# Optimization experiments

Measured on AMD Instinct MI355X. Metric: run time of the kernel, lower is better.

The kernel has to match this reference:

```python
import jax, jax.numpy as jnp
import numpy as np

B, M, N, K = 256, 512, 256, 16


def setup_inputs() -> dict:
    key = jax.random.key(0)
    k1, k2, k3, k4 = jax.random.split(key, 4)
    x = jax.random.normal(k1, (B, M, N), dtype=jnp.float32)
    # Linear(in_features=N, out_features=1): weight [1, N], bias [1]
    w_weight = jax.random.normal(k2, (1, N), dtype=jnp.float32) * (2.0 / (N + 1)) ** 0.5
    w_bias = jnp.zeros((1,), dtype=jnp.float32)
    # v: [N, K], xavier_normal
    v = jax.random.normal(k3, (N, K), dtype=jnp.float32) * (2.0 / (N + K)) ** 0.5
    return {"x": x, "w_weight": w_weight, "w_bias": w_bias, "v": v}


def reference(x, w_weight, w_bias, v):
    # Linear term: [B, M, 1]
    l = x @ w_weight.T + w_bias  # broadcasts bias [1]
    # Pairwise interaction. Original: result[b,a,c] = x[b,a] @ (V V^T) @ x[b,c]
    # p[b,a] = 0.5 * (sum_c result[b,a,c] - result[b,a,a])
    # Efficient O(B*M*K) identity: with xv = x @ V,
    #   sum_c result[b,a,c] = xv[b,a] . sum_c xv[b,c]
    #   result[b,a,a]       = ||xv[b,a]||^2
    xv = jnp.einsum('bmn,nk->bmk', x, v)        # [B, M, K]
    sv = xv.sum(axis=1)                          # [B, K]
    row_sum = jnp.einsum('bmk,bk->bm', xv, sv)  # [B, M]
    diag = jnp.sum(xv * xv, axis=-1)             # [B, M]
    p = 0.5 * (row_sum - diag)                   # [B, M]
    return l + p[..., None]                      # [B, M, 1]
```

## Files before the change

### kernel.cpp

```cpp
#include <hip/hip_runtime.h>

#define B_ 256
#define M_ 512
#define N_ 256
#define K_ 16
#define TR 64
#define NT 4

typedef __attribute__((ext_vector_type(8))) short short8;
typedef __attribute__((ext_vector_type(4))) float f32x4;

__device__ __forceinline__ unsigned short f2bf(float f) {
    unsigned u = __builtin_bit_cast(unsigned, f);
    u += 0x7FFFu + ((u >> 16) & 1u);
    return (unsigned short)(u >> 16);
}
__device__ __forceinline__ float bf2f(unsigned short h) {
    unsigned u = ((unsigned)h) << 16;
    return __builtin_bit_cast(float, u);
}

__global__ __launch_bounds__(256) void fm_pass1(
    const float* __restrict__ x, const float* __restrict__ w,
    const float* __restrict__ bias, const float* __restrict__ v,
    unsigned short* __restrict__ xvb, float* __restrict__ svpart,
    float* __restrict__ out)
{
    __shared__ __align__(16) unsigned char xL[2][TR * 512];
    __shared__ __align__(16) unsigned short wLb[N_];
    __shared__ __align__(16) float red[64];

    const int t   = threadIdx.x;
    const int l   = t & 63;
    const int wv  = t >> 6;
    const int blk = blockIdx.x;
    const int b   = blk >> 1;
    const int m0  = (blk & 1) * (NT * TR);
    const float bias0 = bias[0];

    if (t < 64) {
        float4 wq = *(const float4*)(w + t * 4);
        wLb[t * 4 + 0] = f2bf(wq.x); wLb[t * 4 + 1] = f2bf(wq.y);
        wLb[t * 4 + 2] = f2bf(wq.z); wLb[t * 4 + 3] = f2bf(wq.w);
    }

    short8 vB[8];
    #pragma unroll
    for (int c = 0; c < 8; ++c) {
        #pragma unroll
        for (int j = 0; j < 8; ++j) {
            float f = v[(size_t)(c * 32 + (l >> 4) * 8 + j) * K_ + (l & 15)];
            vB[c][j] = (short)f2bf(f);
        }
    }

    const float* gx = x + (size_t)(b * M_ + m0) * N_;

    const int swq = l >> 1;
    const int shf = (l & 1) * 8;

    float4 st[16];
    #pragma unroll
    for (int j = 0; j < 16; ++j)
        st[j] = *(const float4*)(gx + j * 1024 + t * 4);
    #pragma unroll
    for (int j = 0; j < 16; ++j) {
        const int row = j * 4 + wv;
        unsigned lo = (unsigned)f2bf(st[j].x) | ((unsigned)f2bf(st[j].y) << 16);
        unsigned hi = (unsigned)f2bf(st[j].z) | ((unsigned)f2bf(st[j].w) << 16);
        unsigned* d = (unsigned*)(xL[0] + row * 512 + ((swq ^ (row & 7)) << 4) + shf);
        d[0] = lo; d[1] = hi;
    }
    __syncthreads();

    f32x4 acc[NT];
    #pragma unroll
    for (int T = 0; T < NT; ++T) acc[T] = f32x4{0.f, 0.f, 0.f, 0.f};

    #pragma unroll
    for (int T = 0; T < NT; ++T) {
        const int cur = T & 1;
        if (T + 1 < NT) {
            #pragma unroll
            for (int j = 0; j < 16; ++j)
                st[j] = *(const float4*)(gx + (size_t)(T + 1) * TR * N_ + j * 1024 + t * 4);
        }

        const int arow = wv * 16 + (l & 15);
        const unsigned char* abase = xL[cur] + arow * 512;
        #pragma unroll
        for (int c = 0; c < 8; ++c) {
            short8 a = *(const short8*)(abase + (((c * 4 + (l >> 4)) ^ (arow & 7)) << 4));
            acc[T] = __builtin_amdgcn_mfma_f32_16x16x32_bf16(a, vB[c], acc[T], 0, 0, 0);
        }

        {
            const int row = t >> 2;
            const int qt  = t & 3;
            const unsigned char* rbase = xL[cur] + row * 512;
            float ls = 0.f;
            #pragma unroll
            for (int i = 0; i < 8; ++i) {
                short8 xs = *(const short8*)(rbase + ((((qt * 8 + i)) ^ (row & 7)) << 4));
                short8 ws = *(const short8*)((const unsigned char*)wLb + qt * 128 + i * 16);
                #pragma unroll
                for (int e = 0; e < 8; ++e)
                    ls += bf2f((unsigned short)xs[e]) * bf2f((unsigned short)ws[e]);
            }
            ls += __shfl_xor(ls, 1);
            ls += __shfl_xor(ls, 2);
            if (qt == 0)
                out[(size_t)b * M_ + m0 + T * TR + row] = ls + bias0;
        }

        if (T + 1 < NT) {
            #pragma unroll
            for (int j = 0; j < 16; ++j) {
                const int row = j * 4 + wv;
                unsigned lo = (unsigned)f2bf(st[j].x) | ((unsigned)f2bf(st[j].y) << 16);
                unsigned hi = (unsigned)f2bf(st[j].z) | ((unsigned)f2bf(st[j].w) << 16);
                unsigned* d = (unsigned*)(xL[cur ^ 1] + row * 512 + ((swq ^ (row & 7)) << 4) + shf);
                d[0] = lo; d[1] = hi;
            }
        }
        __syncthreads();
    }

    #pragma unroll
    for (int T = 0; T < NT; ++T) {
        const int rbase = m0 + T * TR + wv * 16 + (l >> 4) * 4;
        #pragma unroll
        for (int r = 0; r < 4; ++r)
            xvb[(size_t)(b * M_ + rbase + r) * K_ + (l & 15)] = f2bf(acc[T][r]);
    }

    float s = 0.f;
    #pragma unroll
    for (int T = 0; T < NT; ++T)
        s += acc[T][0] + acc[T][1] + acc[T][2] + acc[T][3];
    s += __shfl_xor(s, 16);
    s += __shfl_xor(s, 32);
    if (l < 16) red[wv * 16 + l] = s;
    __syncthreads();
    if (t < 16)
        svpart[(size_t)blk * 16 + t] = red[t] + red[16 + t] + red[32 + t] + red[48 + t];
}

__global__ __launch_bounds__(256) void fm_pass2(
    const unsigned short* __restrict__ xvb, const float* __restrict__ svpart,
    float* __restrict__ out)
{
    const int t = threadIdx.x;
    const int blk = blockIdx.x;
    const int b = blk >> 1;
    const int m = (blk & 1) * 256 + t;
    __shared__ __align__(16) float svL[16];
    if (t < 16)
        svL[t] = svpart[(size_t)(b * 2 + 0) * 16 + t] + svpart[(size_t)(b * 2 + 1) * 16 + t];
    __syncthreads();

    const unsigned short* xp = xvb + ((size_t)b * M_ + m) * K_;
    short8 h0 = *(const short8*)(xp);
    short8 h1 = *(const short8*)(xp + 8);

    float rs = 0.f, dg = 0.f;
    #pragma unroll
    for (int k = 0; k < 8; ++k) {
        const float a = bf2f((unsigned short)h0[k]);
        rs += a * svL[k];
        dg += a * a;
    }
    #pragma unroll
    for (int k = 0; k < 8; ++k) {
        const float a = bf2f((unsigned short)h1[k]);
        rs += a * svL[8 + k];
        dg += a * a;
    }

    const size_t o = (size_t)b * M_ + m;
    out[o] = out[o] + 0.5f * (rs - dg);
}

extern "C" void kernel_launch(void* const* d_in, const int* in_sizes, int n_in,
                              void* d_out, int out_size, void* d_ws, size_t ws_size,
                              hipStream_t stream) {
    const float* x    = (const float*)d_in[0];
    const float* w    = (const float*)d_in[1];
    const float* bias = (const float*)d_in[2];
    const float* v    = (const float*)d_in[3];
    float* out = (float*)d_out;

    unsigned short* xvb = (unsigned short*)d_ws;
    float* svpart = (float*)((char*)d_ws + ((size_t)B_ * M_ * K_ * 2));

    fm_pass1<<<dim3(B_ * 2), dim3(256), 0, stream>>>(x, w, bias, v, xvb, svpart, out);
    fm_pass2<<<dim3(B_ * 2), dim3(256), 0, stream>>>(xvb, svpart, out);
}
```

Before: 29.72 us.

## Split pass1 into four blocks per batch with K-split waves and LDS reduction

Pass 1 now launches four blocks per batch instead of two. Each block processes 32-row tiles, and its four waves are arranged as 2 row-groups by 2 N-halves, so each wave runs half the MFMA reduction. The two N-halves' partial xv accumulators are combined through an LDS exchange buffer. The linear-term outputs are held in registers and written after the loop. The goal is more blocks for better CU occupancy and latency hiding, at the cost of an extra sync, extra LDS traffic and more svpart partials that pass 2 must sum.

```diff
diff --git a/kernel.cpp b/kernel.cpp
--- a/kernel.cpp
+++ b/kernel.cpp
@@ -4,8 +4,9 @@
 #define M_ 512
 #define N_ 256
 #define K_ 16
-#define TR 64
+#define TR 32
 #define NT 4
+#define BPB 4
 
 typedef __attribute__((ext_vector_type(8))) short short8;
 typedef __attribute__((ext_vector_type(4))) float f32x4;
@@ -28,14 +29,17 @@
 {
     __shared__ __align__(16) unsigned char xL[2][TR * 512];
     __shared__ __align__(16) unsigned short wLb[N_];
-    __shared__ __align__(16) float red[64];
+    __shared__ __align__(16) float red[32];
+    __shared__ __align__(16) float exch[2 * 64 * 16];
 
     const int t   = threadIdx.x;
     const int l   = t & 63;
     const int wv  = t >> 6;
+    const int wr  = wv & 1;
+    const int wn  = wv >> 1;
     const int blk = blockIdx.x;
-    const int b   = blk >> 1;
-    const int m0  = (blk & 1) * (NT * TR);
+    const int b   = blk >> 2;
+    const int m0  = (blk & 3) * (NT * TR);
     const float bias0 = bias[0];
 
     if (t < 64) {
@@ -44,12 +48,12 @@
         wLb[t * 4 + 2] = f2bf(wq.z); wLb[t * 4 + 3] = f2bf(wq.w);
     }
 
-    short8 vB[8];
-    #pragma unroll
-    for (int c = 0; c < 8; ++c) {
+    short8 vB[4];
+    #pragma unroll
+    for (int c = 0; c < 4; ++c) {
         #pragma unroll
         for (int j = 0; j < 8; ++j) {
-            float f = v[(size_t)(c * 32 + (l >> 4) * 8 + j) * K_ + (l & 15)];
+            float f = v[(size_t)((wn * 4 + c) * 32 + (l >> 4) * 8 + j) * K_ + (l & 15)];
             vB[c][j] = (short)f2bf(f);
         }
     }
@@ -59,12 +63,12 @@
     const int swq = l >> 1;
     const int shf = (l & 1) * 8;
 
-    float4 st[16];
-    #pragma unroll
-    for (int j = 0; j < 16; ++j)
+    float4 st[8];
+    #pragma unroll
+    for (int j = 0; j < 8; ++j)
         st[j] = *(const float4*)(gx + j * 1024 + t * 4);
     #pragma unroll
-    for (int j = 0; j < 16; ++j) {
+    for (int j = 0; j < 8; ++j) {
         const int row = j * 4 + wv;
         unsigned lo = (unsigned)f2bf(st[j].x) | ((unsigned)f2bf(st[j].y) << 16);
         unsigned hi = (unsigned)f2bf(st[j].z) | ((unsigned)f2bf(st[j].w) << 16);
@@ -76,46 +80,49 @@
     f32x4 acc[NT];
     #pragma unroll
     for (int T = 0; T < NT; ++T) acc[T] = f32x4{0.f, 0.f, 0.f, 0.f};
+    float lin[NT];
 
     #pragma unroll
     for (int T = 0; T < NT; ++T) {
         const int cur = T & 1;
         if (T + 1 < NT) {
             #pragma unroll
-            for (int j = 0; j < 16; ++j)
+            for (int j = 0; j < 8; ++j)
                 st[j] = *(const float4*)(gx + (size_t)(T + 1) * TR * N_ + j * 1024 + t * 4);
         }
 
-        const int arow = wv * 16 + (l & 15);
+        const int arow = wr * 16 + (l & 15);
         const unsigned char* abase = xL[cur] + arow * 512;
         #pragma unroll
-        for (int c = 0; c < 8; ++c) {
-            short8 a = *(const short8*)(abase + (((c * 4 + (l >> 4)) ^ (arow & 7)) << 4));
+        for (int c = 0; c < 4; ++c) {
+            const int cq = (wn * 4 + c) * 4 + (l >> 4);
+            short8 a = *(const short8*)(abase + ((cq ^ (arow & 7)) << 4));
             acc[T] = __builtin_amdgcn_mfma_f32_16x16x32_bf16(a, vB[c], acc[T], 0, 0, 0);
         }
 
         {
-            const int row = t >> 2;
-            const int qt  = t & 3;
+            const int row = t >> 3;
+            const int qt  = t & 7;
             const unsigned char* rbase = xL[cur] + row * 512;
             float ls = 0.f;
             #pragma unroll
-            for (int i = 0; i < 8; ++i) {
-                short8 xs = *(const short8*)(rbase + ((((qt * 8 + i)) ^ (row & 7)) << 4));
-                short8 ws = *(const short8*)((const unsigned char*)wLb + qt * 128 + i * 16);
+            for (int i = 0; i < 4; ++i) {
+                const int qi = qt * 4 + i;
+                short8 xs = *(const short8*)(rbase + ((qi ^ (row & 7)) << 4));
+                short8 ws = *(const short8*)((const unsigned char*)wLb + qi * 16);
                 #pragma unroll
                 for (int e = 0; e < 8; ++e)
                     ls += bf2f((unsigned short)xs[e]) * bf2f((unsigned short)ws[e]);
             }
             ls += __shfl_xor(ls, 1);
             ls += __shfl_xor(ls, 2);
-            if (qt == 0)
-                out[(size_t)b * M_ + m0 + T * TR + row] = ls + bias0;
+            ls += __shfl_xor(ls, 4);
+            lin[T] = ls;
         }
 
         if (T + 1 < NT) {
             #pragma unroll
-            for (int j = 0; j < 16; ++j) {
+            for (int j = 0; j < 8; ++j) {
                 const int row = j * 4 + wv;
                 unsigned lo = (unsigned)f2bf(st[j].x) | ((unsigned)f2bf(st[j].y) << 16);
                 unsigned hi = (unsigned)f2bf(st[j].z) | ((unsigned)f2bf(st[j].w) << 16);
@@ -126,24 +133,49 @@
         __syncthreads();
     }
 
-    #pragma unroll
-    for (int T = 0; T < NT; ++T) {
-        const int rbase = m0 + T * TR + wv * 16 + (l >> 4) * 4;
-        #pragma unroll
-        for (int r = 0; r < 4; ++r)
-            xvb[(size_t)(b * M_ + rbase + r) * K_ + (l & 15)] = f2bf(acc[T][r]);
-    }
-
-    float s = 0.f;
-    #pragma unroll
-    for (int T = 0; T < NT; ++T)
-        s += acc[T][0] + acc[T][1] + acc[T][2] + acc[T][3];
-    s += __shfl_xor(s, 16);
-    s += __shfl_xor(s, 32);
-    if (l < 16) red[wv * 16 + l] = s;
+    if ((t & 7) == 0) {
+        #pragma unroll
+        for (int T = 0; T < NT; ++T)
+            out[(size_t)b * M_ + m0 + T * TR + (t >> 3)] = lin[T] + bias0;
+    }
+
+    {
+        float* dst = exch + (size_t)(wr * 64 + l) * 16;
+        if (wn == 1) {
+            #pragma unroll
+            for (int T = 0; T < NT; ++T)
+                *(f32x4*)(dst + T * 4) = acc[T];
+        }
+    }
+    __syncthreads();
+    if (wn == 0) {
+        const float* src = exch + (size_t)(wr * 64 + l) * 16;
+        #pragma unroll
+        for (int T = 0; T < NT; ++T) {
+            f32x4 o = *(const f32x4*)(src + T * 4);
+            acc[T][0] += o[0]; acc[T][1] += o[1];
+            acc[T][2] += o[2]; acc[T][3] += o[3];
+        }
+
+        #pragma unroll
+        for (int T = 0; T < NT; ++T) {
+            const int rbase = m0 + T * TR + wr * 16 + (l >> 4) * 4;
+            #pragma unroll
+            for (int r = 0; r < 4; ++r)
+                xvb[(size_t)(b * M_ + rbase + r) * K_ + (l & 15)] = f2bf(acc[T][r]);
+        }
+
+        float s = 0.f;
+        #pragma unroll
+        for (int T = 0; T < NT; ++T)
+            s += acc[T][0] + acc[T][1] + acc[T][2] + acc[T][3];
+        s += __shfl_xor(s, 16);
+        s += __shfl_xor(s, 32);
+        if (l < 16) red[wr * 16 + l] = s;
+    }
     __syncthreads();
     if (t < 16)
-        svpart[(size_t)blk * 16 + t] = red[t] + red[16 + t] + red[32 + t] + red[48 + t];
+        svpart[(size_t)blk * 16 + t] = red[t] + red[16 + t];
 }
 
 __global__ __launch_bounds__(256) void fm_pass2(
@@ -155,8 +187,13 @@
     const int b = blk >> 1;
     const int m = (blk & 1) * 256 + t;
     __shared__ __align__(16) float svL[16];
-    if (t < 16)
-        svL[t] = svpart[(size_t)(b * 2 + 0) * 16 + t] + svpart[(size_t)(b * 2 + 1) * 16 + t];
+    if (t < 16) {
+        float s = 0.f;
+        #pragma unroll
+        for (int j = 0; j < BPB; ++j)
+            s += svpart[(size_t)(b * BPB + j) * 16 + t];
+        svL[t] = s;
+    }
     __syncthreads();
 
     const unsigned short* xp = xvb + ((size_t)b * M_ + m) * K_;
@@ -193,6 +230,6 @@
     unsigned short* xvb = (unsigned short*)d_ws;
     float* svpart = (float*)((char*)d_ws + ((size_t)B_ * M_ * K_ * 2));
 
-    fm_pass1<<<dim3(B_ * 2), dim3(256), 0, stream>>>(x, w, bias, v, xvb, svpart, out);
+    fm_pass1<<<dim3(B_ * BPB), dim3(256), 0, stream>>>(x, w, bias, v, xvb, svpart, out);
     fm_pass2<<<dim3(B_ * 2), dim3(256), 0, stream>>>(xvb, svpart, out);
 }
```

After: 29.76 us. Within noise of the previous version (+0.1%).
